# Kernel optimization log

Hardware: AMD Instinct MI355X
Metric: run time of the kernel (lower is better)

The kernel has to match this reference:

```python
import jax, jax.numpy as jnp
import numpy as np

N0, N1, N2, F, H, O, B = 1_000_000, 200_000, 40_000, 128, 64, 64, 1024
EPS = 1e-5


def _bn(h, g, b):
    # BatchNorm1d, training mode: biased batch statistics over the node dim
    m = h.mean(0)
    v = jnp.mean(jnp.square(h - m), 0)
    return (h - m) * jax.lax.rsqrt(v + EPS) * g + b


def _mlp(h, Wa, ba, ga, bea, Wb, bb, gb, beb):
    h = jax.nn.relu(_bn(h @ Wa + ba, ga, bea))
    h = jax.nn.relu(_bn(h @ Wb + bb, gb, beb))
    return h


def _conv(x, src, dst, n_out, params):
    # scatter-add aggregation: out[dst] += x[src]  (flow=target_to_source, aggr=add)
    agg = jax.ops.segment_sum(x[src], dst, num_segments=n_out)
    return _mlp(agg, *params)


def setup_inputs() -> dict:
    key = jax.random.key(0)
    ks = jax.random.split(key, 12)

    def lin(k, i, o):
        return (jax.random.normal(k, (i, o), jnp.float32) / np.sqrt(i)).astype(jnp.float32)

    d = {}
    d["x"] = jax.random.normal(ks[0], (N0, F), jnp.float32)
    d["e1_dst"] = jax.random.randint(ks[1], (N0,), 0, N1, jnp.int32)
    d["e1_src"] = jnp.arange(N0, dtype=jnp.int32)
    d["e2_dst"] = jax.random.randint(ks[2], (N1,), 0, N2, jnp.int32)
    d["e2_src"] = jnp.arange(N1, dtype=jnp.int32)
    d["batch1"] = jnp.sort(jax.random.randint(ks[3], (N1,), 0, B, jnp.int32))
    d["batch2"] = jnp.sort(jax.random.randint(ks[4], (N2,), 0, B, jnp.int32))
    # conv1 MLP params
    d["W1a"] = lin(ks[5], F, H); d["b1a"] = jnp.zeros((H,), jnp.float32)
    d["g1a"] = jnp.ones((H,), jnp.float32); d["be1a"] = jnp.zeros((H,), jnp.float32)
    d["W1b"] = lin(ks[6], H, H); d["b1b"] = jnp.zeros((H,), jnp.float32)
    d["g1b"] = jnp.ones((H,), jnp.float32); d["be1b"] = jnp.zeros((H,), jnp.float32)
    # conv2 MLP params
    d["W2a"] = lin(ks[7], H, H); d["b2a"] = jnp.zeros((H,), jnp.float32)
    d["g2a"] = jnp.ones((H,), jnp.float32); d["be2a"] = jnp.zeros((H,), jnp.float32)
    d["W2b"] = lin(ks[8], H, H); d["b2b"] = jnp.zeros((H,), jnp.float32)
    d["g2b"] = jnp.ones((H,), jnp.float32); d["be2b"] = jnp.zeros((H,), jnp.float32)
    # dim_align: Linear(nhid*num_convs, output_dim), dropout p=0 -> identity
    d["Wout"] = lin(ks[9], 2 * H, O); d["bout"] = jnp.zeros((O,), jnp.float32)
    d["num_graphs"] = B
    return d


def reference(x, e1_dst, e1_src, e2_dst, e2_src, batch1, batch2,
              W1a, b1a, g1a, be1a, W1b, b1b, g1b, be1b,
              W2a, b2a, g2a, be2a, W2b, b2b, g2b, be2b,
              Wout, bout, num_graphs):
    n1 = batch1.shape[0]
    n2 = batch2.shape[0]
    x1 = _conv(x, e1_src, e1_dst, n1, (W1a, b1a, g1a, be1a, W1b, b1b, g1b, be1b))
    x2 = _conv(x1, e2_src, e2_dst, n2, (W2a, b2a, g2a, be2a, W2b, b2b, g2b, be2b))
    # global sum pooling per layer, then concat and dim_align
    p1 = jax.ops.segment_sum(x1, batch1, num_segments=num_graphs)
    p2 = jax.ops.segment_sum(x2, batch2, num_segments=num_graphs)
    pooled = jnp.concatenate([p1, p2], axis=1)  # [B, 2H]
    return pooled @ Wout + bout
```

## Files before the change

kernel.cpp:

```cpp
#include <hip/hip_runtime.h>

#define N0 1000000
#define N1 200000
#define N2 40000
#define FDIM 128
#define HDIM 64
#define ODIM 64
#define NB 1024
#define EPSV 1e-5f
#define GCHUNK 64
#define NGW1 15625
#define NCHUNK1 196
#define NREP 32

__global__ __launch_bounds__(256) void k_hist(const int* __restrict__ dst,
                                              int* __restrict__ deg, int E)
{
  int i = blockIdx.x * 256 + threadIdx.x;
  const int stride = gridDim.x * 256;
  for (; i < E; i += stride) atomicAdd(&deg[dst[i]], 1);
}

__global__ __launch_bounds__(256) void k_scanA(const int* __restrict__ deg,
                                               int* __restrict__ csum, int M)
{
  __shared__ int red[256];
  const int b = blockIdx.x, t = threadIdx.x;
  const int base = b * 1024 + t * 4;
  int s = 0;
#pragma unroll
  for (int j = 0; j < 4; ++j) {
    int i = base + j;
    if (i < M) s += deg[i];
  }
  red[t] = s;
  __syncthreads();
  for (int off = 128; off > 0; off >>= 1) {
    if (t < off) red[t] += red[t + off];
    __syncthreads();
  }
  if (t == 0) csum[b] = red[0];
}

__global__ __launch_bounds__(256) void k_scanC(const int* __restrict__ deg,
                                               const int* __restrict__ csum,
                                               int* __restrict__ off,
                                               int* __restrict__ cur,
                                               int M, int nchunk)
{
  __shared__ int red[256];
  __shared__ int top[256];
  const int b = blockIdx.x, t = threadIdx.x;
  top[t] = (t < nchunk) ? csum[t] : 0;
  const int base = b * 1024 + t * 4;
  int v[4];
  int s = 0;
#pragma unroll
  for (int j = 0; j < 4; ++j) {
    int i = base + j;
    v[j] = (i < M) ? deg[i] : 0;
    s += v[j];
  }
  red[t] = s;
  __syncthreads();
  for (int o = 1; o < 256; o <<= 1) {
    int addR = (t >= o) ? red[t - o] : 0;
    int addT = (t >= o) ? top[t - o] : 0;
    __syncthreads();
    red[t] += addR;
    top[t] += addT;
    __syncthreads();
  }
  const int cbase = (b == 0) ? 0 : top[b - 1];
  int start = cbase + red[t] - s;
#pragma unroll
  for (int j = 0; j < 4; ++j) {
    int i = base + j;
    if (i < M) { off[i] = start; cur[i] = start; }
    start += v[j];
  }
  if (b == nchunk - 1 && t == 255) off[M] = start;
}

__global__ __launch_bounds__(256) void k_fill(const int* __restrict__ dst,
                                              int* __restrict__ cur,
                                              int* __restrict__ eidx, int E)
{
  int i = blockIdx.x * 256 + threadIdx.x;
  const int stride = gridDim.x * 256;
  for (; i < E; i += stride) {
    int p = atomicAdd(&cur[dst[i]], 1);
    eidx[p] = i;
  }
}

__device__ __forceinline__ int lowerb(const int* __restrict__ a, int n, int v)
{
  int lo = 0, hi = n;
  while (lo < hi) {
    int mid = (lo + hi) >> 1;
    if (a[mid] < v) lo = mid + 1; else hi = mid;
  }
  return lo;
}

__global__ __launch_bounds__(256) void k_wstart(const int* __restrict__ off,
                                                int* __restrict__ ws,
                                                int M, int ngw)
{
  int w = blockIdx.x * 256 + threadIdx.x;
  if (w < ngw) ws[w] = lowerb(off, M + 1, w * GCHUNK);
}

__global__ __launch_bounds__(128) void k_conv1(
    const float* __restrict__ x, const int* __restrict__ off,
    const int* __restrict__ ws, const int* __restrict__ eidx,
    const float* __restrict__ W, float* __restrict__ out,
    float* __restrict__ stats)
{
  __shared__ __align__(16) float xs[FDIM];
  __shared__ float ps[2][2][HDIM];
  __shared__ __align__(16) int ids[2][GCHUNK];
  const int lane = threadIdx.x & 63;
  const int hf = threadIdx.x >> 6;
  const int wid = blockIdx.x;
  const int d0 = ws[wid];
  const int d1 = (wid == NGW1 - 1) ? N1 : ws[wid + 1];
  if (d0 >= d1) return;
  float w[HDIM];
#pragma unroll
  for (int k = 0; k < HDIM; ++k) w[k] = W[(hf * HDIM + k) * HDIM + lane];
  const float* xh = x + hf * HDIM + lane;
  const int e_start = off[d0];
  const int e_end = off[d1];
  int d = d0;
  int nend = off[d0 + 1];
  int parity = 0;
  float acc = 0.f;
  float ss = 0.f, qq = 0.f;

  auto FLUSH = [&]() {
    xs[hf * HDIM + lane] = acc;
    float p0 = 0.f, p1 = 0.f, p2 = 0.f, p3 = 0.f;
#pragma unroll
    for (int kk = 0; kk < HDIM; kk += 4) {
      float4 xv = *(const float4*)&xs[hf * HDIM + kk];
      p0 = fmaf(xv.x, w[kk + 0], p0);
      p1 = fmaf(xv.y, w[kk + 1], p1);
      p2 = fmaf(xv.z, w[kk + 2], p2);
      p3 = fmaf(xv.w, w[kk + 3], p3);
    }
    ps[parity][hf][lane] = (p0 + p1) + (p2 + p3);
    asm volatile("s_waitcnt lgkmcnt(0)" ::: "memory");
    __builtin_amdgcn_s_barrier();
    if (hf == 0) {
      float h = ps[parity][0][lane] + ps[parity][1][lane];
      out[(size_t)d * HDIM + lane] = h;
      ss += h;
      qq += h * h;
    }
    parity ^= 1;
    acc = 0.f;
    ++d;
    nend = off[min(d + 1, N1)];
  };

  int j = e_start;
  while (j < e_end) {
    const int cnt = min(64, e_end - j);
    ids[hf][lane] = eidx[min(j + lane, N0 - 1)];
    int k = 0;
    float vA[8];
    if (k + 8 <= cnt) {
#pragma unroll
      for (int u = 0; u < 8; ++u) vA[u] = xh[(size_t)ids[hf][u] * FDIM];
    }
    while (k + 8 <= cnt) {
      const bool more = (k + 16 <= cnt);
      float vB[8];
      if (more) {
#pragma unroll
        for (int u = 0; u < 8; ++u)
          vB[u] = xh[(size_t)ids[hf][k + 8 + u] * FDIM];
      }
#pragma unroll
      for (int u = 0; u < 8; ++u) {
        while (j + k + u == nend) FLUSH();
        acc += vA[u];
      }
      if (more) {
#pragma unroll
        for (int u = 0; u < 8; ++u) vA[u] = vB[u];
      }
      k += 8;
    }
    for (; k < cnt; ++k) {
      float v0 = xh[(size_t)ids[hf][k] * FDIM];
      while (j + k == nend) FLUSH();
      acc += v0;
    }
    j += cnt;
  }
  while (d < d1) FLUSH();

  if (hf == 0) {
    float* rep = stats + (size_t)(wid & (NREP - 1)) * 2 * HDIM;
    unsafeAtomicAdd(&rep[lane], ss);
    unsafeAtomicAdd(&rep[HDIM + lane], qq);
  }
}

template <bool BNIN, bool STATS>
__global__ __launch_bounds__(256) void k_gemm64(
    const float* __restrict__ in, int M, const float* __restrict__ W,
    const float* __restrict__ sumsIn, int nrep, const float* __restrict__ g,
    const float* __restrict__ be, float invN,
    float* __restrict__ out, float* __restrict__ osum, float* __restrict__ osq)
{
  __shared__ __align__(16) float xs[4][HDIM * 4];
  __shared__ float AC[2][HDIM];
  const int lane = threadIdx.x & 63;
  const int wv = threadIdx.x >> 6;
  if constexpr (BNIN) {
    if (threadIdx.x < 64) {
      float sm = 0.f, sq = 0.f;
      for (int r = 0; r < nrep; ++r) {
        sm += sumsIn[r * 2 * HDIM + threadIdx.x];
        sq += sumsIn[r * 2 * HDIM + HDIM + threadIdx.x];
      }
      float m = sm * invN;
      float var = sq * invN - m * m;
      float a = rsqrtf(var + EPSV) * g[threadIdx.x];
      AC[0][threadIdx.x] = a;
      AC[1][threadIdx.x] = be[threadIdx.x] - m * a;
    }
    __syncthreads();
  }
  float w[HDIM];
#pragma unroll
  for (int k = 0; k < HDIM; ++k) w[k] = W[k * HDIM + lane];
  const int r = lane >> 4;
  const int seg = lane & 15;
  float4 av = make_float4(1.f, 1.f, 1.f, 1.f);
  float4 cv = make_float4(0.f, 0.f, 0.f, 0.f);
  if constexpr (BNIN) {
    av = *(const float4*)&AC[0][seg * 4];
    cv = *(const float4*)&AC[1][seg * 4];
  }
  float ss = 0.f, qq = 0.f;
  const int sweep = gridDim.x * 16;
  for (int base = (blockIdx.x * 4 + wv) * 4; base < M; base += sweep) {
    float4 v = *(const float4*)(in + (size_t)(base + r) * HDIM + seg * 4);
    if constexpr (BNIN) {
      v.x = fmaxf(0.f, fmaf(v.x, av.x, cv.x));
      v.y = fmaxf(0.f, fmaf(v.y, av.y, cv.y));
      v.z = fmaxf(0.f, fmaf(v.z, av.z, cv.z));
      v.w = fmaxf(0.f, fmaf(v.w, av.w, cv.w));
    }
    const int k0 = seg * 4;
    xs[wv][(k0 + 0) * 4 + r] = v.x;
    xs[wv][(k0 + 1) * 4 + r] = v.y;
    xs[wv][(k0 + 2) * 4 + r] = v.z;
    xs[wv][(k0 + 3) * 4 + r] = v.w;
    float a0 = 0.f, a1 = 0.f, a2 = 0.f, a3 = 0.f;
#pragma unroll
    for (int k = 0; k < HDIM; ++k) {
      float4 xv = *(const float4*)&xs[wv][k * 4];
      a0 = fmaf(xv.x, w[k], a0);
      a1 = fmaf(xv.y, w[k], a1);
      a2 = fmaf(xv.z, w[k], a2);
      a3 = fmaf(xv.w, w[k], a3);
    }
    out[(size_t)(base + 0) * HDIM + lane] = a0;
    out[(size_t)(base + 1) * HDIM + lane] = a1;
    out[(size_t)(base + 2) * HDIM + lane] = a2;
    out[(size_t)(base + 3) * HDIM + lane] = a3;
    if constexpr (STATS) {
      ss += a0 + a1 + a2 + a3;
      qq += a0 * a0 + a1 * a1 + a2 * a2 + a3 * a3;
    }
  }
  if constexpr (STATS) {
    __shared__ float red[2][4][HDIM];
    red[0][wv][lane] = ss;
    red[1][wv][lane] = qq;
    __syncthreads();
    if (wv == 0) {
      float s = red[0][0][lane] + red[0][1][lane] + red[0][2][lane] + red[0][3][lane];
      float q = red[1][0][lane] + red[1][1][lane] + red[1][2][lane] + red[1][3][lane];
      unsafeAtomicAdd(&osum[lane], s);
      unsafeAtomicAdd(&osq[lane], q);
    }
  }
}

template <bool SCATTER>
__global__ __launch_bounds__(256) void k_bnrelu_pool(
    const float* __restrict__ in, const float* __restrict__ sumsIn,
    const float* __restrict__ g, const float* __restrict__ be, float invN,
    const int* __restrict__ dst, float* __restrict__ agg,
    const int* __restrict__ batch, float* __restrict__ pool, int M)
{
  const int lane = threadIdx.x & 63;
  const int wv = threadIdx.x >> 6;
  const int nw = gridDim.x * 4;
  const int wid = blockIdx.x * 4 + wv;
  const int chunk = (M + nw - 1) / nw;
  int r0 = wid * chunk;
  int r1 = min(M, r0 + chunk);
  if (r0 >= r1) return;
  const float m = sumsIn[lane] * invN;
  const float var = sumsIn[64 + lane] * invN - m * m;
  const float a = rsqrtf(var + EPSV) * g[lane];
  const float c = be[lane] - m * a;
  int curb = batch[r0];
  float pacc = 0.f;
  for (int row = r0; row < r1; ++row) {
    float v = fmaxf(0.f, fmaf(in[(size_t)row * HDIM + lane], a, c));
    if constexpr (SCATTER)
      unsafeAtomicAdd(&agg[(size_t)dst[row] * HDIM + lane], v);
    int b = batch[row];
    if (b != curb) {
      unsafeAtomicAdd(&pool[(size_t)curb * HDIM + lane], pacc);
      pacc = 0.f;
      curb = b;
    }
    pacc += v;
  }
  unsafeAtomicAdd(&pool[(size_t)curb * HDIM + lane], pacc);
}

__global__ __launch_bounds__(256) void k_final(
    const float* __restrict__ p1, const float* __restrict__ p2,
    const float* __restrict__ Wout, const float* __restrict__ bo,
    float* __restrict__ out)
{
  const int row = blockIdx.x * 4 + (threadIdx.x >> 6);
  const int j = threadIdx.x & 63;
  const float* q1 = p1 + (size_t)row * HDIM;
  const float* q2 = p2 + (size_t)row * HDIM;
  float acc = bo[j];
#pragma unroll
  for (int k = 0; k < HDIM; ++k) acc = fmaf(q1[k], Wout[k * ODIM + j], acc);
#pragma unroll
  for (int k = 0; k < HDIM; ++k) acc = fmaf(q2[k], Wout[(HDIM + k) * ODIM + j], acc);
  out[(size_t)row * ODIM + j] = acc;
}

extern "C" void kernel_launch(void* const* d_in, const int* in_sizes, int n_in,
                              void* d_out, int out_size, void* d_ws, size_t ws_size,
                              hipStream_t stream)
{
  (void)in_sizes; (void)n_in; (void)out_size; (void)ws_size;
  const float* x      = (const float*)d_in[0];
  const int*  e1_dst  = (const int*)d_in[1];
  const int*  e2_dst  = (const int*)d_in[3];
  const int*  batch1  = (const int*)d_in[5];
  const int*  batch2  = (const int*)d_in[6];
  const float* W1a  = (const float*)d_in[7];
  const float* g1a  = (const float*)d_in[9];
  const float* be1a = (const float*)d_in[10];
  const float* W1b  = (const float*)d_in[11];
  const float* g1b  = (const float*)d_in[13];
  const float* be1b = (const float*)d_in[14];
  const float* W2a  = (const float*)d_in[15];
  const float* g2a  = (const float*)d_in[17];
  const float* be2a = (const float*)d_in[18];
  const float* W2b  = (const float*)d_in[19];
  const float* g2b  = (const float*)d_in[21];
  const float* be2b = (const float*)d_in[22];
  const float* Wout = (const float*)d_in[23];
  const float* bout = (const float*)d_in[24];

  float* ws = (float*)d_ws;
  float* h1pre = ws;
  float* h2pre = h1pre + (size_t)N1 * HDIM;
  float* agg2  = h2pre + (size_t)N1 * HDIM;
  float* h3pre = agg2 + (size_t)N2 * HDIM;
  float* h4pre = h3pre + (size_t)N2 * HDIM;
  float* p1    = h4pre + (size_t)N2 * HDIM;
  float* p2    = p1 + (size_t)NB * HDIM;
  float* st1   = p2 + (size_t)NB * HDIM;
  float* st2   = st1 + NREP * 2 * HDIM;
  float* st3   = st2 + 2 * HDIM;
  float* st4   = st3 + 2 * HDIM;
  int* deg1  = (int*)(st4 + 2 * HDIM);
  int* off1  = deg1 + N1;
  int* cur1  = off1 + N1 + 1;
  int* csum1 = cur1 + N1;
  int* eidx1 = csum1 + 256;
  int* ws1   = eidx1 + N0;

  hipMemsetAsync(deg1, 0, (size_t)N1 * sizeof(int), stream);
  hipMemsetAsync(agg2, 0, (size_t)N2 * HDIM * sizeof(float), stream);
  hipMemsetAsync(p1, 0,
                 (2 * (size_t)NB * HDIM + (NREP + 3) * 2 * HDIM) * sizeof(float),
                 stream);

  k_hist<<<1024, 256, 0, stream>>>(e1_dst, deg1, N0);
  k_scanA<<<NCHUNK1, 256, 0, stream>>>(deg1, csum1, N1);
  k_scanC<<<NCHUNK1, 256, 0, stream>>>(deg1, csum1, off1, cur1, N1, NCHUNK1);
  k_fill<<<1024, 256, 0, stream>>>(e1_dst, cur1, eidx1, N0);
  k_wstart<<<(NGW1 + 255) / 256, 256, 0, stream>>>(off1, ws1, N1, NGW1);

  k_conv1<<<NGW1, 128, 0, stream>>>(x, off1, ws1, eidx1, W1a, h1pre, st1);
  k_gemm64<true, true><<<1024, 256, 0, stream>>>(
      h1pre, N1, W1b, st1, NREP, g1a, be1a, 1.f / N1, h2pre,
      st2, st2 + HDIM);
  k_bnrelu_pool<true><<<1024, 256, 0, stream>>>(
      h2pre, st2, g1b, be1b, 1.f / N1, e2_dst, agg2, batch1, p1, N1);
  k_gemm64<false, true><<<512, 256, 0, stream>>>(
      agg2, N2, W2a, nullptr, 0, nullptr, nullptr, 0.f, h3pre,
      st3, st3 + HDIM);
  k_gemm64<true, true><<<512, 256, 0, stream>>>(
      h3pre, N2, W2b, st3, 1, g2a, be2a, 1.f / N2, h4pre,
      st4, st4 + HDIM);
  k_bnrelu_pool<false><<<512, 256, 0, stream>>>(
      h4pre, st4, g2b, be2b, 1.f / N2, nullptr, nullptr, batch2, p2, N2);
  k_final<<<NB / 4, 256, 0, stream>>>(p1, p2, Wout, bout, (float*)d_out);
}
```

Before: 474.5 us.

## Prefetch conv1 offsets/indices into LDS, deepen gather pipeline, fuse fill with wstart

Merges the fill and window-start kernels into one launch, removing a kernel boundary. In conv1, each block preloads up to 80 CSR offsets and 96 edge indices into shared memory once, replacing per-chunk eidx loads and per-flush global off reads. The gather loop becomes a three-stage register pipeline (vA/vB/vC) for deeper memory-level parallelism. Indices past the cached range fall back to global loads, and the extra registers may lower occupancy.

Result: slower. 704.4 us (+48.5%).

```diff
diff --git a/kernel.cpp b/kernel.cpp
--- a/kernel.cpp
+++ b/kernel.cpp
@@ -12,6 +12,8 @@
 #define NGW1 15625
 #define NCHUNK1 196
 #define NREP 32
+#define NIDS 96
+#define NOFFS 80
 
 __global__ __launch_bounds__(256) void k_hist(const int* __restrict__ dst,
                                               int* __restrict__ deg, int E)
@@ -82,18 +84,6 @@
   if (b == nchunk - 1 && t == 255) off[M] = start;
 }
 
-__global__ __launch_bounds__(256) void k_fill(const int* __restrict__ dst,
-                                              int* __restrict__ cur,
-                                              int* __restrict__ eidx, int E)
-{
-  int i = blockIdx.x * 256 + threadIdx.x;
-  const int stride = gridDim.x * 256;
-  for (; i < E; i += stride) {
-    int p = atomicAdd(&cur[dst[i]], 1);
-    eidx[p] = i;
-  }
-}
-
 __device__ __forceinline__ int lowerb(const int* __restrict__ a, int n, int v)
 {
   int lo = 0, hi = n;
@@ -104,12 +94,17 @@
   return lo;
 }
 
-__global__ __launch_bounds__(256) void k_wstart(const int* __restrict__ off,
-                                                int* __restrict__ ws,
-                                                int M, int ngw)
-{
-  int w = blockIdx.x * 256 + threadIdx.x;
-  if (w < ngw) ws[w] = lowerb(off, M + 1, w * GCHUNK);
+__global__ __launch_bounds__(256) void k_fill_ws(
+    const int* __restrict__ dst, int* __restrict__ cur, int* __restrict__ eidx,
+    int E, const int* __restrict__ off, int* __restrict__ ws, int M, int ngw)
+{
+  const int stride = gridDim.x * 256;
+  for (int i = blockIdx.x * 256 + threadIdx.x; i < E; i += stride) {
+    int p = atomicAdd(&cur[dst[i]], 1);
+    eidx[p] = i;
+  }
+  for (int w = blockIdx.x * 256 + threadIdx.x; w < ngw; w += stride)
+    ws[w] = lowerb(off, M + 1, w * GCHUNK);
 }
 
 __global__ __launch_bounds__(128) void k_conv1(
@@ -120,25 +115,35 @@
 {
   __shared__ __align__(16) float xs[FDIM];
   __shared__ float ps[2][2][HDIM];
-  __shared__ __align__(16) int ids[2][GCHUNK];
+  __shared__ __align__(16) int ids[2][NIDS];
+  __shared__ int offs[2][NOFFS];
   const int lane = threadIdx.x & 63;
   const int hf = threadIdx.x >> 6;
   const int wid = blockIdx.x;
   const int d0 = ws[wid];
   const int d1 = (wid == NGW1 - 1) ? N1 : ws[wid + 1];
   if (d0 >= d1) return;
+  offs[hf][lane] = off[min(d0 + lane, N1)];
+  if (lane < NOFFS - 64) offs[hf][64 + lane] = off[min(d0 + 64 + lane, N1)];
+  const int e_start = offs[hf][0];
+  const int e_end = (d1 - d0 < NOFFS) ? offs[hf][d1 - d0] : off[d1];
+  const int cnt = e_end - e_start;
+  ids[hf][lane] = eidx[min(e_start + lane, N0 - 1)];
+  if (lane < NIDS - 64)
+    ids[hf][64 + lane] = eidx[min(e_start + 64 + lane, N0 - 1)];
   float w[HDIM];
 #pragma unroll
   for (int k = 0; k < HDIM; ++k) w[k] = W[(hf * HDIM + k) * HDIM + lane];
   const float* xh = x + hf * HDIM + lane;
-  const int e_start = off[d0];
-  const int e_end = off[d1];
   int d = d0;
-  int nend = off[d0 + 1];
+  int nend = offs[hf][1];
   int parity = 0;
   float acc = 0.f;
   float ss = 0.f, qq = 0.f;
 
+  auto IDX = [&](int jj) -> int {
+    return (jj < NIDS) ? ids[hf][jj] : eidx[e_start + jj];
+  };
   auto FLUSH = [&]() {
     xs[hf * HDIM + lane] = acc;
     float p0 = 0.f, p1 = 0.f, p2 = 0.f, p3 = 0.f;
@@ -162,44 +167,34 @@
     parity ^= 1;
     acc = 0.f;
     ++d;
-    nend = off[min(d + 1, N1)];
+    int idx = d + 1 - d0;
+    nend = (idx < NOFFS) ? offs[hf][idx] : off[min(d + 1, N1)];
   };
-
-  int j = e_start;
-  while (j < e_end) {
-    const int cnt = min(64, e_end - j);
-    ids[hf][lane] = eidx[min(j + lane, N0 - 1)];
-    int k = 0;
-    float vA[8];
-    if (k + 8 <= cnt) {
-#pragma unroll
-      for (int u = 0; u < 8; ++u) vA[u] = xh[(size_t)ids[hf][u] * FDIM];
-    }
-    while (k + 8 <= cnt) {
-      const bool more = (k + 16 <= cnt);
-      float vB[8];
-      if (more) {
-#pragma unroll
-        for (int u = 0; u < 8; ++u)
-          vB[u] = xh[(size_t)ids[hf][k + 8 + u] * FDIM];
-      }
-#pragma unroll
-      for (int u = 0; u < 8; ++u) {
-        while (j + k + u == nend) FLUSH();
-        acc += vA[u];
-      }
-      if (more) {
-#pragma unroll
-        for (int u = 0; u < 8; ++u) vA[u] = vB[u];
-      }
-      k += 8;
-    }
-    for (; k < cnt; ++k) {
-      float v0 = xh[(size_t)ids[hf][k] * FDIM];
-      while (j + k == nend) FLUSH();
-      acc += v0;
-    }
-    j += cnt;
+  auto LOAD8 = [&](float* v, int base) {
+#pragma unroll
+    for (int u = 0; u < 8; ++u) v[u] = xh[(size_t)IDX(base + u) * FDIM];
+  };
+
+  const int n8 = cnt & ~7;
+  float vA[8], vB[8], vC[8];
+  if (n8 >= 8) LOAD8(vA, 0);
+  if (n8 >= 16) LOAD8(vB, 8);
+  int k = 0;
+  while (k + 8 <= n8) {
+    if (k + 24 <= n8) LOAD8(vC, k + 16);
+#pragma unroll
+    for (int u = 0; u < 8; ++u) {
+      while (e_start + k + u == nend) FLUSH();
+      acc += vA[u];
+    }
+#pragma unroll
+    for (int u = 0; u < 8; ++u) { vA[u] = vB[u]; vB[u] = vC[u]; }
+    k += 8;
+  }
+  for (; k < cnt; ++k) {
+    float v0 = xh[(size_t)IDX(k) * FDIM];
+    while (e_start + k == nend) FLUSH();
+    acc += v0;
   }
   while (d < d1) FLUSH();
 
@@ -400,8 +395,8 @@
   k_hist<<<1024, 256, 0, stream>>>(e1_dst, deg1, N0);
   k_scanA<<<NCHUNK1, 256, 0, stream>>>(deg1, csum1, N1);
   k_scanC<<<NCHUNK1, 256, 0, stream>>>(deg1, csum1, off1, cur1, N1, NCHUNK1);
-  k_fill<<<1024, 256, 0, stream>>>(e1_dst, cur1, eidx1, N0);
-  k_wstart<<<(NGW1 + 255) / 256, 256, 0, stream>>>(off1, ws1, N1, NGW1);
+  k_fill_ws<<<1024, 256, 0, stream>>>(e1_dst, cur1, eidx1, N0, off1, ws1, N1,
+                                      NGW1);
 
   k_conv1<<<NGW1, 128, 0, stream>>>(x, off1, ws1, eidx1, W1a, h1pre, st1);
   k_gemm64<true, true><<<1024, 256, 0, stream>>>(
```
